# Performance work log

Measured on AMD Instinct MI355X. Metric: run time of the kernel, lower is better.

Reference implementation:

```python
import jax, jax.numpy as jnp
import numpy as np

N_NODES = 50000
N_EDGES = 800000
D_FEAT = 256
HIDDEN = 256
N_CLASSES = 10
N_GRAPHS = 128


def setup_inputs() -> dict:
    key = jax.random.key(0)
    ks = jax.random.split(key, 16)
    x = jax.random.normal(ks[0], (N_NODES, D_FEAT), dtype=jnp.float32)
    edge_index = jax.random.randint(ks[1], (2, N_EDGES), 0, N_NODES, dtype=jnp.int64)
    batch = jnp.sort(jax.random.randint(ks[2], (N_NODES,), 0, N_GRAPHS, dtype=jnp.int64))
    def lin(k, fin, fout):
        s = 1.0 / np.sqrt(fin)
        return jax.random.uniform(k, (fin, fout), jnp.float32, -s, s)
    return {
        "x": x, "edge_index": edge_index, "batch": batch,
        "W0": lin(ks[3], D_FEAT, HIDDEN), "b0": jnp.zeros((HIDDEN,), jnp.float32),
        "W1": lin(ks[4], HIDDEN, HIDDEN), "b1": jnp.zeros((HIDDEN,), jnp.float32),
        "W2": lin(ks[5], HIDDEN, HIDDEN), "b2": jnp.zeros((HIDDEN,), jnp.float32),
        "fc1_W": lin(ks[6], HIDDEN, HIDDEN), "fc1_b": jnp.zeros((HIDDEN,), jnp.float32),
        "fc2_W": lin(ks[7], HIDDEN, N_CLASSES), "fc2_b": jnp.zeros((N_CLASSES,), jnp.float32),
    }


def _gcn_norm(edge_index, n_nodes):
    # PyG GCNConv: add self-loops, deg from (A+I) with unit weights,
    # norm_e = deg^{-1/2}[src] * deg^{-1/2}[dst]
    loop = jnp.arange(n_nodes, dtype=edge_index.dtype)
    src = jnp.concatenate([edge_index[0], loop])
    dst = jnp.concatenate([edge_index[1], loop])
    deg = jax.ops.segment_sum(jnp.ones_like(dst, dtype=jnp.float32), dst,
                              num_segments=n_nodes)
    dinv = jnp.where(deg > 0, jax.lax.rsqrt(deg), 0.0)
    norm = dinv[src] * dinv[dst]
    return src, dst, norm


def _gcn_conv(x, src, dst, norm, W, b, n_nodes):
    h = x @ W                              # [N, out]
    msg = h[src] * norm[:, None]           # gather + scale  [E+N, out]
    out = jax.ops.segment_sum(msg, dst, num_segments=n_nodes)  # scatter-add
    return out + b


def reference(x, edge_index, batch, W0, b0, W1, b1, W2, b2, fc1_W, fc1_b, fc2_W, fc2_b):
    n_nodes = x.shape[0]
    src, dst, norm = _gcn_norm(edge_index, n_nodes)
    h = jax.nn.relu(_gcn_conv(x, src, dst, norm, W0, b0, n_nodes))
    h = jax.nn.relu(_gcn_conv(h, src, dst, norm, W1, b1, n_nodes))
    h = jax.nn.relu(_gcn_conv(h, src, dst, norm, W2, b2, n_nodes))
    # global add pool over graphs
    g = jax.ops.segment_sum(h, batch, num_segments=N_GRAPHS)   # [G, H]
    g = jax.nn.relu(g @ fc1_W + fc1_b)
    # dropout p=0.5 is identity in eval mode
    logits = g @ fc2_W + fc2_b
    return jax.nn.log_softmax(logits, axis=-1)
```

## Files before the change

### kernel.cpp

```cpp
#include <hip/hip_runtime.h>
#include <math.h>

#define FDIM 256
#define NGRAPH 128
#define NCLASS 10

typedef short short8 __attribute__((ext_vector_type(8)));
typedef float floatx4 __attribute__((ext_vector_type(4)));

static __device__ __forceinline__ unsigned short f2bf(float f) {
    unsigned u = __float_as_uint(f);
    u += 0x7FFF + ((u >> 16) & 1);
    return (unsigned short)(u >> 16);
}


__global__ __launch_bounds__(256) void prep_kernel(const int* __restrict__ dst,
                                                   int* __restrict__ cnt,
                                                   unsigned short* __restrict__ slot,
                                                   int E, int nCnt,
                                                   const float* __restrict__ W0,
                                                   const float* __restrict__ W1,
                                                   const float* __restrict__ W2,
                                                   unsigned short* __restrict__ Bp0,
                                                   unsigned short* __restrict__ Bp1,
                                                   unsigned short* __restrict__ Bp2,
                                                   float4* __restrict__ g4) {
    const int b = blockIdx.x;
    const int t = threadIdx.x;
    if (b < nCnt) {
        int e = b * 256 + t;
        if (e < E) slot[e] = (unsigned short)atomicAdd(&cnt[dst[e]], 1);
        return;
    }
    const int b2 = b - nCnt;
    if (b2 >= 96) {
        g4[(size_t)(b2 - 96) * 256 + t] = (float4){0.f, 0.f, 0.f, 0.f};
        return;
    }
    const float* W = (b2 < 32) ? W0 : (b2 < 64) ? W1 : W2;
    unsigned short* Bp = (b2 < 32) ? Bp0 : (b2 < 64) ? Bp1 : Bp2;
    int idx = (b2 & 31) * 256 + t;
    int kstep = idx >> 10;
    int ntile = (idx >> 6) & 15;
    int lane  = idx & 63;
    int col   = ntile * 16 + (lane & 15);
    int krow  = kstep * 32 + (lane >> 4) * 8;
    unsigned short o[8];
#pragma unroll
    for (int j = 0; j < 8; j++) o[j] = f2bf(W[(size_t)(krow + j) * FDIM + col]);
    *(uint4*)(Bp + (size_t)idx * 8) = *(uint4*)o;
}


__global__ __launch_bounds__(256) void csr_bsum(const int* __restrict__ cnt,
                                                int* __restrict__ bsum, int N) {
    __shared__ int red[256];
    const int t = threadIdx.x;
    const int base = blockIdx.x * 1024 + t * 4;
    int s = 0;
#pragma unroll
    for (int i = 0; i < 4; i++)
        if (base + i < N) s += cnt[base + i];
    red[t] = s;
    __syncthreads();
    for (int off = 128; off > 0; off >>= 1) {
        if (t < off) red[t] += red[t + off];
        __syncthreads();
    }
    if (t == 0) bsum[blockIdx.x] = red[0];
}

__global__ __launch_bounds__(256) void csr_scan2(const int* __restrict__ cnt,
                                                 const int* __restrict__ bsum,
                                                 int* __restrict__ rowptr,
                                                 float* __restrict__ dinv, int N, int E) {
    __shared__ int redo[256];
    __shared__ int tsum[256];
    const int t = threadIdx.x;
    const int bid = blockIdx.x;

    int pre = 0;
    for (int i = t; i < bid; i += 256) pre += bsum[i];
    redo[t] = pre;
    __syncthreads();
    for (int off = 128; off > 0; off >>= 1) {
        if (t < off) redo[t] += redo[t + off];
        __syncthreads();
    }
    const int blockoff = redo[0];
    __syncthreads();

    const int base = bid * 1024 + t * 4;
    int c[4];
    int s = 0;
#pragma unroll
    for (int i = 0; i < 4; i++) {
        c[i] = (base + i < N) ? cnt[base + i] : 0;
        s += c[i];
    }
    tsum[t] = s;
    __syncthreads();
    for (int off = 1; off < 256; off <<= 1) {
        int v = (t >= off) ? tsum[t - off] : 0;
        __syncthreads();
        tsum[t] += v;
        __syncthreads();
    }
    int run = blockoff + ((t == 0) ? 0 : tsum[t - 1]);
#pragma unroll
    for (int i = 0; i < 4; i++) {
        int idx = base + i;
        if (idx < N) {
            rowptr[idx] = run;
            dinv[idx] = rsqrtf((float)c[i] + 1.0f);
            run += c[i];
        }
    }
    if (bid == 0 && t == 0) rowptr[N] = E;
}


static __device__ __forceinline__ void gemm_tile16_f32(const float* __restrict__ A,
                                                       const unsigned short* __restrict__ Bp,
                                                       unsigned short* __restrict__ C,
                                                       int M, int tile) {
    const int wave = threadIdx.x >> 6;
    const int lane = threadIdx.x & 63;
    const int quad = lane >> 4;
    const int m    = lane & 15;
    const int row0 = tile * 64 + wave * 16;

    const int r0 = min(row0 + m, M - 1);
    const float* arow = A + (size_t)r0 * FDIM + quad * 8;

    floatx4 acc[16];
#pragma unroll
    for (int i = 0; i < 16; i++) acc[i] = (floatx4){0.f, 0.f, 0.f, 0.f};

#pragma unroll
    for (int kstep = 0; kstep < 8; kstep++) {
        float4 p0 = *(const float4*)(arow + kstep * 32);
        float4 p1 = *(const float4*)(arow + kstep * 32 + 4);
        short8 a;
        a[0] = (short)f2bf(p0.x); a[1] = (short)f2bf(p0.y);
        a[2] = (short)f2bf(p0.z); a[3] = (short)f2bf(p0.w);
        a[4] = (short)f2bf(p1.x); a[5] = (short)f2bf(p1.y);
        a[6] = (short)f2bf(p1.z); a[7] = (short)f2bf(p1.w);
#pragma unroll
        for (int nt = 0; nt < 16; nt++) {
            short8 b = *(const short8*)((const short*)Bp +
                         ((size_t)(kstep * 16 + nt) * 64 + lane) * 8);
            acc[nt] = __builtin_amdgcn_mfma_f32_16x16x32_bf16(a, b, acc[nt], 0, 0, 0);
        }
    }
#pragma unroll
    for (int nt = 0; nt < 16; nt++) {
        int col = nt * 16 + m;
#pragma unroll
        for (int r = 0; r < 4; r++) {
            int row = row0 + quad * 4 + r;
            if (row < M) C[(size_t)row * FDIM + col] = f2bf(acc[nt][r]);
        }
    }
}

__global__ __launch_bounds__(256) void gemm0_fill_kernel(const float* __restrict__ x,
                                                         const unsigned short* __restrict__ Bp0,
                                                         unsigned short* __restrict__ H,
                                                         int M, int ng,
                                                         const int* __restrict__ src,
                                                         const int* __restrict__ dst,
                                                         const int* __restrict__ rowptr,
                                                         const unsigned short* __restrict__ slot,
                                                         unsigned short* __restrict__ srcs, int E) {
    if ((int)blockIdx.x < ng) {
        gemm_tile16_f32(x, Bp0, H, M, blockIdx.x);
        return;
    }
    int e = (blockIdx.x - ng) * 256 + threadIdx.x;
    if (e < E) srcs[rowptr[dst[e]] + (int)slot[e]] = (unsigned short)src[e];
}

__global__ __launch_bounds__(256) void mfma_gemm(const unsigned short* __restrict__ A,
                                                 const unsigned short* __restrict__ Bp,
                                                 unsigned short* __restrict__ C, int M) {
    const int wave = threadIdx.x >> 6;
    const int lane = threadIdx.x & 63;
    const int quad = lane >> 4;
    const int m    = lane & 15;
    const int row0 = blockIdx.x * 64 + wave * 16;

    const short* arow = (const short*)A + (size_t)(row0 + m) * FDIM + quad * 8;

    floatx4 acc[16];
#pragma unroll
    for (int i = 0; i < 16; i++) acc[i] = (floatx4){0.f, 0.f, 0.f, 0.f};

#pragma unroll
    for (int kstep = 0; kstep < 8; kstep++) {
        short8 a = *(const short8*)(arow + kstep * 32);
#pragma unroll
        for (int nt = 0; nt < 16; nt++) {
            short8 b = *(const short8*)((const short*)Bp +
                         ((size_t)(kstep * 16 + nt) * 64 + lane) * 8);
            acc[nt] = __builtin_amdgcn_mfma_f32_16x16x32_bf16(a, b, acc[nt], 0, 0, 0);
        }
    }
#pragma unroll
    for (int nt = 0; nt < 16; nt++) {
        int col = nt * 16 + m;
#pragma unroll
        for (int r = 0; r < 4; r++) {
            int row = row0 + quad * 4 + r;
            if (row < M) C[(size_t)row * FDIM + col] = f2bf(acc[nt][r]);
        }
    }
}


static __device__ __forceinline__ void accum8(float* acc, uint4 v, float nm) {
    const unsigned* u = (const unsigned*)&v;
#pragma unroll
    for (int i = 0; i < 4; i++) {
        acc[2 * i]     += nm * __uint_as_float(u[i] << 16);
        acc[2 * i + 1] += nm * __uint_as_float(u[i] & 0xFFFF0000u);
    }
}

static __device__ __forceinline__ void gather_node(const unsigned short* __restrict__ h,
                                                   const int* __restrict__ rowptr,
                                                   const unsigned short* __restrict__ srcs,
                                                   const float* __restrict__ dinv,
                                                   const float* __restrict__ bias,
                                                   int node, int lane, float* acc) {
    const float di = dinv[node];
    {
        uint4 sv = *(const uint4*)(h + (size_t)node * FDIM + lane * 8);
        const unsigned* u = (const unsigned*)&sv;
#pragma unroll
        for (int i = 0; i < 4; i++) {
            acc[2 * i]     = di * di * __uint_as_float(u[i] << 16);
            acc[2 * i + 1] = di * di * __uint_as_float(u[i] & 0xFFFF0000u);
        }
        float4 b0 = *(const float4*)(bias + lane * 8);
        float4 b1 = *(const float4*)(bias + lane * 8 + 4);
        acc[0] += b0.x; acc[1] += b0.y; acc[2] += b0.z; acc[3] += b0.w;
        acc[4] += b1.x; acc[5] += b1.y; acc[6] += b1.z; acc[7] += b1.w;
    }
    const int beg = rowptr[node];
    const int end = rowptr[node + 1];
    int p = beg;
    for (; p + 4 <= end; p += 4) {
        int s0 = srcs[p], s1 = srcs[p + 1], s2 = srcs[p + 2], s3 = srcs[p + 3];
        float n0 = dinv[s0] * di, n1 = dinv[s1] * di;
        float n2 = dinv[s2] * di, n3 = dinv[s3] * di;
        uint4 v0 = *(const uint4*)(h + (size_t)s0 * FDIM + lane * 8);
        uint4 v1 = *(const uint4*)(h + (size_t)s1 * FDIM + lane * 8);
        uint4 v2 = *(const uint4*)(h + (size_t)s2 * FDIM + lane * 8);
        uint4 v3 = *(const uint4*)(h + (size_t)s3 * FDIM + lane * 8);
        accum8(acc, v0, n0);
        accum8(acc, v1, n1);
        accum8(acc, v2, n2);
        accum8(acc, v3, n3);
    }
    for (; p < end; p++) {
        int s = srcs[p];
        float nm = dinv[s] * di;
        uint4 v = *(const uint4*)(h + (size_t)s * FDIM + lane * 8);
        accum8(acc, v, nm);
    }
#pragma unroll
    for (int i = 0; i < 8; i++) acc[i] = fmaxf(acc[i], 0.0f);
}

__global__ __launch_bounds__(256) void gather_kernel(const unsigned short* __restrict__ h,
                                                     const int* __restrict__ rowptr,
                                                     const unsigned short* __restrict__ srcs,
                                                     const float* __restrict__ dinv,
                                                     const float* __restrict__ bias,
                                                     unsigned short* __restrict__ out, int N) {
    const int node = blockIdx.x * 8 + (threadIdx.x >> 5);
    const int lane = threadIdx.x & 31;
    if (node >= N) return;
    float acc[8];
    gather_node(h, rowptr, srcs, dinv, bias, node, lane, acc);
    unsigned short o[8];
#pragma unroll
    for (int i = 0; i < 8; i++) o[i] = f2bf(acc[i]);
    *(uint4*)(out + (size_t)node * FDIM + lane * 8) = *(uint4*)o;
}

__global__ __launch_bounds__(256) void gather_pool_kernel(const unsigned short* __restrict__ h,
                                                          const int* __restrict__ rowptr,
                                                          const unsigned short* __restrict__ srcs,
                                                          const float* __restrict__ dinv,
                                                          const float* __restrict__ bias,
                                                          const int* __restrict__ batch,
                                                          float* __restrict__ g, int N) {
    __shared__ float red[8][FDIM];
    __shared__ int bid[8];
    const int hw   = threadIdx.x >> 5;
    const int lane = threadIdx.x & 31;
    const int node = blockIdx.x * 8 + hw;

    float acc[8] = {0.f, 0.f, 0.f, 0.f, 0.f, 0.f, 0.f, 0.f};
    if (node < N) gather_node(h, rowptr, srcs, dinv, bias, node, lane, acc);
#pragma unroll
    for (int i = 0; i < 8; i++) red[hw][lane * 8 + i] = acc[i];
    if (lane == 0) bid[hw] = (node < N) ? batch[node] : -1;
    __syncthreads();

    const int f = threadIdx.x;
    int cur = -1;
    float run = 0.0f;
    for (int i = 0; i < 8; i++) {
        int b = bid[i];
        if (b < 0) break;
        if (b != cur) {
            if (cur >= 0) atomicAdd(&g[(size_t)cur * FDIM + f], run);
            cur = b;
            run = 0.0f;
        }
        run += red[i][f];
    }
    if (cur >= 0) atomicAdd(&g[(size_t)cur * FDIM + f], run);
}


__global__ __launch_bounds__(256) void fc_head_kernel(const float* __restrict__ g,
                                                      const float* __restrict__ fc1W,
                                                      const float* __restrict__ fc1b,
                                                      const float* __restrict__ fc2W,
                                                      const float* __restrict__ fc2b,
                                                      float* __restrict__ out) {
    __shared__ float gs[FDIM];
    __shared__ float part[4][FDIM];
    __shared__ float hs[FDIM];
    __shared__ float p2[256];
    __shared__ float logits[NCLASS];
    const int r = blockIdx.x;
    const int t = threadIdx.x;
    const int w = t >> 6;
    const int l = t & 63;

    gs[t] = g[(size_t)r * FDIM + t];
    __syncthreads();

    float a[4] = {0.f, 0.f, 0.f, 0.f};
    for (int kk = 0; kk < 64; kk++) {
        int k = w * 64 + kk;
        float gv = gs[k];
#pragma unroll
        for (int j = 0; j < 4; j++) a[j] += gv * fc1W[(size_t)k * FDIM + j * 64 + l];
    }
#pragma unroll
    for (int j = 0; j < 4; j++) part[w][j * 64 + l] = a[j];
    __syncthreads();

    float s1 = part[0][t] + part[1][t] + part[2][t] + part[3][t] + fc1b[t];
    hs[t] = fmaxf(s1, 0.0f);
    __syncthreads();

    float a2 = 0.0f;
    const int c = t & 15;
    if (c < NCLASS) {
        int k0 = (t >> 4) * 16;
        for (int kk = 0; kk < 16; kk++)
            a2 += hs[k0 + kk] * fc2W[(size_t)(k0 + kk) * NCLASS + c];
    }
    p2[t] = a2;
    __syncthreads();

    if (t < NCLASS) {
        float s2 = fc2b[t];
        for (int seg = 0; seg < 16; seg++) s2 += p2[seg * 16 + t];
        logits[t] = s2;
    }
    __syncthreads();

    if (t == 0) {
        float mx = logits[0];
        for (int cc = 1; cc < NCLASS; cc++) mx = fmaxf(mx, logits[cc]);
        float ssum = 0.0f;
        for (int cc = 0; cc < NCLASS; cc++) ssum += expf(logits[cc] - mx);
        float lse = mx + logf(ssum);
        for (int cc = 0; cc < NCLASS; cc++) out[(size_t)r * NCLASS + cc] = logits[cc] - lse;
    }
}


extern "C" void kernel_launch(void* const* d_in, const int* in_sizes, int n_in,
                              void* d_out, int out_size, void* d_ws, size_t ws_size,
                              hipStream_t stream) {
    const float* x     = (const float*)d_in[0];
    const int*   ei    = (const int*)d_in[1];
    const int*   batch = (const int*)d_in[2];
    const float* W0 = (const float*)d_in[3];  const float* b0 = (const float*)d_in[4];
    const float* W1 = (const float*)d_in[5];  const float* b1 = (const float*)d_in[6];
    const float* W2 = (const float*)d_in[7];  const float* b2 = (const float*)d_in[8];
    const float* fc1W = (const float*)d_in[9];  const float* fc1b = (const float*)d_in[10];
    const float* fc2W = (const float*)d_in[11]; const float* fc2b = (const float*)d_in[12];
    float* out = (float*)d_out;

    const int N = in_sizes[0] / FDIM;
    const int E = in_sizes[1] / 2;
    const int* src = ei;
    const int* dst = ei + E;
    const int Mpad = ((N + 63) / 64) * 64;
    const int nb   = (N + 1023) / 1024;
    const int nCnt = (E + 255) / 256;
    const int ng   = (N + 63) / 64;

    char* p = (char*)d_ws;
    unsigned short* S  = (unsigned short*)p; p += (size_t)Mpad * FDIM * 2;
    unsigned short* H  = (unsigned short*)p; p += (size_t)Mpad * FDIM * 2;
    unsigned short* Wp0 = (unsigned short*)p; p += (size_t)8192 * 8 * 2;
    unsigned short* Wp1 = (unsigned short*)p; p += (size_t)8192 * 8 * 2;
    unsigned short* Wp2 = (unsigned short*)p; p += (size_t)8192 * 8 * 2;
    float* dinv = (float*)p; p += (size_t)N * 4;
    int*   cnt  = (int*)p;   p += (size_t)N * 4;
    int*   rowptr = (int*)p; p += (size_t)(N + 4) * 4;
    int*   bsum = (int*)p;   p += (size_t)256 * 4;
    unsigned short* srcs = (unsigned short*)p; p += (((size_t)E * 2 + 15) & ~15ull);
    unsigned short* slot = (unsigned short*)p; p += (((size_t)E * 2 + 15) & ~15ull);
    float* g    = (float*)p;

    hipMemsetAsync(cnt, 0, (size_t)N * sizeof(int), stream);
    prep_kernel<<<nCnt + 128, 256, 0, stream>>>(dst, cnt, slot, E, nCnt,
                                                W0, W1, W2, Wp0, Wp1, Wp2, (float4*)g);
    csr_bsum<<<nb, 256, 0, stream>>>(cnt, bsum, N);
    csr_scan2<<<nb, 256, 0, stream>>>(cnt, bsum, rowptr, dinv, N, E);

    gemm0_fill_kernel<<<ng + nCnt, 256, 0, stream>>>(x, Wp0, H, N, ng,
                                                     src, dst, rowptr, slot, srcs, E);

    gather_kernel<<<(N + 7) / 8, 256, 0, stream>>>(H, rowptr, srcs, dinv, b0, S, N);
    mfma_gemm<<<ng, 256, 0, stream>>>(S, Wp1, H, N);
    gather_kernel<<<(N + 7) / 8, 256, 0, stream>>>(H, rowptr, srcs, dinv, b1, S, N);
    mfma_gemm<<<ng, 256, 0, stream>>>(S, Wp2, H, N);
    gather_pool_kernel<<<(N + 7) / 8, 256, 0, stream>>>(H, rowptr, srcs, dinv, b2,
                                                        batch, g, N);
    fc_head_kernel<<<NGRAPH, 256, 0, stream>>>(g, fc1W, fc1b, fc2W, fc2b, out);
}
```

Measured before the change: 443.0 us.

## Hold B fragments in registers per wave and loop over row tiles

The GEMM tile is reorganised so each wave owns a 64-column slice of the output and keeps all its B fragments (8 k-steps × 4 column tiles) in registers, then iterates over four 16-row M sub-tiles. Before, every wave streamed the entire 256-column B matrix from memory for its own 16 rows. The aim is to cut the repeated B loads (L2/L1 traffic) four-fold per block. In exchange each wave loads the A rows of all 64 rows (4x more A loads per wave, mostly from cache), register pressure rises from the 128-VGPR breg array, and the launch bound is set to 2 blocks per SM.

```diff
diff --git a/kernel.cpp b/kernel.cpp
--- a/kernel.cpp
+++ b/kernel.cpp
@@ -121,101 +121,82 @@
 }
 
 
-static __device__ __forceinline__ void gemm_tile16_f32(const float* __restrict__ A,
-                                                       const unsigned short* __restrict__ Bp,
-                                                       unsigned short* __restrict__ C,
-                                                       int M, int tile) {
+template<int AFP32>
+static __device__ __forceinline__ void gemm_tile64(const void* __restrict__ A,
+                                                   const unsigned short* __restrict__ Bp,
+                                                   unsigned short* __restrict__ C,
+                                                   int M, int tile) {
     const int wave = threadIdx.x >> 6;
     const int lane = threadIdx.x & 63;
     const int quad = lane >> 4;
     const int m    = lane & 15;
-    const int row0 = tile * 64 + wave * 16;
-
-    const int r0 = min(row0 + m, M - 1);
-    const float* arow = A + (size_t)r0 * FDIM + quad * 8;
-
-    floatx4 acc[16];
-#pragma unroll
-    for (int i = 0; i < 16; i++) acc[i] = (floatx4){0.f, 0.f, 0.f, 0.f};
-
-#pragma unroll
-    for (int kstep = 0; kstep < 8; kstep++) {
-        float4 p0 = *(const float4*)(arow + kstep * 32);
-        float4 p1 = *(const float4*)(arow + kstep * 32 + 4);
-        short8 a;
-        a[0] = (short)f2bf(p0.x); a[1] = (short)f2bf(p0.y);
-        a[2] = (short)f2bf(p0.z); a[3] = (short)f2bf(p0.w);
-        a[4] = (short)f2bf(p1.x); a[5] = (short)f2bf(p1.y);
-        a[6] = (short)f2bf(p1.z); a[7] = (short)f2bf(p1.w);
-#pragma unroll
-        for (int nt = 0; nt < 16; nt++) {
-            short8 b = *(const short8*)((const short*)Bp +
-                         ((size_t)(kstep * 16 + nt) * 64 + lane) * 8);
-            acc[nt] = __builtin_amdgcn_mfma_f32_16x16x32_bf16(a, b, acc[nt], 0, 0, 0);
+    const int row0 = tile * 64;
+
+    short8 breg[8][4];
+#pragma unroll
+    for (int ks = 0; ks < 8; ks++)
+#pragma unroll
+        for (int j = 0; j < 4; j++)
+            breg[ks][j] = *(const short8*)((const short*)Bp +
+                            ((size_t)((ks * 16 + wave * 4 + j) * 64 + lane) * 8));
+
+#pragma unroll
+    for (int mt = 0; mt < 4; mt++) {
+        const int r0 = min(row0 + mt * 16 + m, M - 1);
+        floatx4 acc[4];
+#pragma unroll
+        for (int j = 0; j < 4; j++) acc[j] = (floatx4){0.f, 0.f, 0.f, 0.f};
+#pragma unroll
+        for (int ks = 0; ks < 8; ks++) {
+            short8 a;
+            if (AFP32) {
+                const float* ar = (const float*)A + (size_t)r0 * FDIM + ks * 32 + quad * 8;
+                float4 p0 = *(const float4*)ar;
+                float4 p1 = *(const float4*)(ar + 4);
+                a[0] = (short)f2bf(p0.x); a[1] = (short)f2bf(p0.y);
+                a[2] = (short)f2bf(p0.z); a[3] = (short)f2bf(p0.w);
+                a[4] = (short)f2bf(p1.x); a[5] = (short)f2bf(p1.y);
+                a[6] = (short)f2bf(p1.z); a[7] = (short)f2bf(p1.w);
+            } else {
+                a = *(const short8*)((const short*)A + (size_t)r0 * FDIM + ks * 32 + quad * 8);
+            }
+#pragma unroll
+            for (int j = 0; j < 4; j++)
+                acc[j] = __builtin_amdgcn_mfma_f32_16x16x32_bf16(a, breg[ks][j], acc[j], 0, 0, 0);
         }
-    }
-#pragma unroll
-    for (int nt = 0; nt < 16; nt++) {
-        int col = nt * 16 + m;
-#pragma unroll
-        for (int r = 0; r < 4; r++) {
-            int row = row0 + quad * 4 + r;
-            if (row < M) C[(size_t)row * FDIM + col] = f2bf(acc[nt][r]);
+#pragma unroll
+        for (int j = 0; j < 4; j++) {
+            int col = (wave * 4 + j) * 16 + m;
+#pragma unroll
+            for (int r = 0; r < 4; r++) {
+                int row = row0 + mt * 16 + quad * 4 + r;
+                if (row < M) C[(size_t)row * FDIM + col] = f2bf(acc[j][r]);
+            }
         }
     }
 }
 
-__global__ __launch_bounds__(256) void gemm0_fill_kernel(const float* __restrict__ x,
-                                                         const unsigned short* __restrict__ Bp0,
-                                                         unsigned short* __restrict__ H,
-                                                         int M, int ng,
-                                                         const int* __restrict__ src,
-                                                         const int* __restrict__ dst,
-                                                         const int* __restrict__ rowptr,
-                                                         const unsigned short* __restrict__ slot,
-                                                         unsigned short* __restrict__ srcs, int E) {
+__global__ __launch_bounds__(256, 2) void gemm0_fill_kernel(const float* __restrict__ x,
+                                                            const unsigned short* __restrict__ Bp0,
+                                                            unsigned short* __restrict__ H,
+                                                            int M, int ng,
+                                                            const int* __restrict__ src,
+                                                            const int* __restrict__ dst,
+                                                            const int* __restrict__ rowptr,
+                                                            const unsigned short* __restrict__ slot,
+                                                            unsigned short* __restrict__ srcs, int E) {
     if ((int)blockIdx.x < ng) {
-        gemm_tile16_f32(x, Bp0, H, M, blockIdx.x);
+        gemm_tile64<1>(x, Bp0, H, M, blockIdx.x);
         return;
     }
     int e = (blockIdx.x - ng) * 256 + threadIdx.x;
     if (e < E) srcs[rowptr[dst[e]] + (int)slot[e]] = (unsigned short)src[e];
 }
 
-__global__ __launch_bounds__(256) void mfma_gemm(const unsigned short* __restrict__ A,
-                                                 const unsigned short* __restrict__ Bp,
-                                                 unsigned short* __restrict__ C, int M) {
-    const int wave = threadIdx.x >> 6;
-    const int lane = threadIdx.x & 63;
-    const int quad = lane >> 4;
-    const int m    = lane & 15;
-    const int row0 = blockIdx.x * 64 + wave * 16;
-
-    const short* arow = (const short*)A + (size_t)(row0 + m) * FDIM + quad * 8;
-
-    floatx4 acc[16];
-#pragma unroll
-    for (int i = 0; i < 16; i++) acc[i] = (floatx4){0.f, 0.f, 0.f, 0.f};
-
-#pragma unroll
-    for (int kstep = 0; kstep < 8; kstep++) {
-        short8 a = *(const short8*)(arow + kstep * 32);
-#pragma unroll
-        for (int nt = 0; nt < 16; nt++) {
-            short8 b = *(const short8*)((const short*)Bp +
-                         ((size_t)(kstep * 16 + nt) * 64 + lane) * 8);
-            acc[nt] = __builtin_amdgcn_mfma_f32_16x16x32_bf16(a, b, acc[nt], 0, 0, 0);
-        }
-    }
-#pragma unroll
-    for (int nt = 0; nt < 16; nt++) {
-        int col = nt * 16 + m;
-#pragma unroll
-        for (int r = 0; r < 4; r++) {
-            int row = row0 + quad * 4 + r;
-            if (row < M) C[(size_t)row * FDIM + col] = f2bf(acc[nt][r]);
-        }
-    }
+__global__ __launch_bounds__(256, 2) void mfma_gemm(const unsigned short* __restrict__ A,
+                                                    const unsigned short* __restrict__ Bp,
+                                                    unsigned short* __restrict__ C, int M) {
+    gemm_tile64<0>(A, Bp, C, M, blockIdx.x);
 }
 
 
```

New measurement: 421.9 us. -4.7%, faster.
